# Kernel tuning notes

Hardware: AMD Instinct MI355X
Metric: run time of the kernel (lower is better)

The kernel has to match this reference:

```python
import jax, jax.numpy as jnp
import numpy as np

B, H, S_MAX, D = 2, 32, 8192, 128
S_NEW = 512

def setup_inputs() -> dict:
    key = jax.random.key(0)
    k1, k2 = jax.random.split(key)
    return {
        "input_pos": jnp.arange(S_NEW, dtype=jnp.int64 if jax.config.jax_enable_x64 else jnp.int32),
        "k_val": jax.random.normal(k1, (B, H, S_NEW, D), dtype=jnp.float32),
        "v_val": jax.random.normal(k2, (B, H, S_NEW, D), dtype=jnp.float32),
        "k_cache": jnp.zeros((B, H, S_MAX, D), dtype=jnp.float32),
        "kt_cache": jnp.zeros((B, H, D, S_MAX), dtype=jnp.float32),
        "v_cache": jnp.zeros((B, H, S_MAX, D), dtype=jnp.float32),
    }

def reference(input_pos, k_val, v_val, k_cache, kt_cache, v_cache):
    # Scatter-write new K/V (and K^T) into the caches at input_pos.
    k_out = k_cache.at[:, :, input_pos].set(k_val)                      # [B,H,S_max,D]
    kt_out = kt_cache.at[:, :, :, input_pos].set(
        jnp.swapaxes(k_val, -1, -2))                                    # [B,H,D,S_max]
    v_out = v_cache.at[:, :, input_pos].set(v_val)                      # [B,H,S_max,D]
    # Module returns (kt.transpose(-1,-2), k, v)
    return (jnp.swapaxes(kt_out, -1, -2), k_out, v_out)
```

## Files before the change

kernel.cpp:

```cpp
#include <hip/hip_runtime.h>


#define S_MAXC 8192
#define DC     128
#define BHC    64

__global__ void init_inv(int* __restrict__ inv) {
    int i = blockIdx.x * blockDim.x + threadIdx.x;
    if (i < S_MAXC) inv[i] = -1;
}

__global__ void scatter_inv(const int* __restrict__ pos, int* __restrict__ inv, int n) {
    int j = blockIdx.x * blockDim.x + threadIdx.x;
    if (j < n) inv[pos[j]] = j;
}

__global__ void __launch_bounds__(256) copy_scatter(
        const float4* __restrict__ k_val,
        const float4* __restrict__ v_val,
        const float4* __restrict__ k_cache,
        const float4* __restrict__ v_cache,
        const int*    __restrict__ inv,
        float4* __restrict__ out_k,
        float4* __restrict__ out_v,
        int s_new) {
    long i = (long)blockIdx.x * blockDim.x + threadIdx.x;
    int d4 = (int)(i & 31);
    int s  = (int)((i >> 5) & (S_MAXC - 1));
    int bh = (int)(i >> 18);
    int j = inv[s];
    if (j >= 0) {
        long src = ((long)bh * s_new + j) * 32 + d4;
        out_k[i] = k_val[src];
        out_v[i] = v_val[src];
    } else {
        out_k[i] = k_cache[i];
        out_v[i] = v_cache[i];
    }
}

__global__ void __launch_bounds__(256) transpose_kt(
        const float*  __restrict__ kt_cache,
        const float4* __restrict__ k_val,
        const int*    __restrict__ inv,
        float4* __restrict__ out0,
        int s_new) {
    __shared__ __align__(16) float tile[32][132];
    const int bh = blockIdx.y;
    const int s0 = blockIdx.x * 32;
    const int t  = threadIdx.x;
    const int q  = t & 7;
    const int r  = t >> 3;

    const float* ktb = kt_cache + (long)bh * DC * S_MAXC;
    #pragma unroll
    for (int p = 0; p < 4; ++p) {
        int d = p * 32 + r;
        float4 vld = *(const float4*)(ktb + (long)d * S_MAXC + s0 + 4 * q);
        tile[4 * q + 0][d] = vld.x;
        tile[4 * q + 1][d] = vld.y;
        tile[4 * q + 2][d] = vld.z;
        tile[4 * q + 3][d] = vld.w;
    }
    __syncthreads();

    const int sl = r;
    const int s  = s0 + sl;
    const int j  = inv[s];
    float4* outrow = out0 + ((long)bh * S_MAXC + s) * 32;
    if (j >= 0) {
        const float4* src = k_val + ((long)bh * s_new + j) * 32;
        #pragma unroll
        for (int m = 0; m < 4; ++m)
            outrow[q + 8 * m] = src[q + 8 * m];
    } else {
        #pragma unroll
        for (int m = 0; m < 4; ++m) {
            int dd = 4 * (q + 8 * m);
            outrow[q + 8 * m] = *(const float4*)&tile[sl][dd];
        }
    }
}

extern "C" void kernel_launch(void* const* d_in, const int* in_sizes, int n_in,
                              void* d_out, int out_size, void* d_ws, size_t ws_size,
                              hipStream_t stream) {
    const int*   input_pos = (const int*)  d_in[0];
    const float* k_val     = (const float*)d_in[1];
    const float* v_val     = (const float*)d_in[2];
    const float* k_cache   = (const float*)d_in[3];
    const float* kt_cache  = (const float*)d_in[4];
    const float* v_cache   = (const float*)d_in[5];
    const int s_new = in_sizes[0];

    const long per_out = (long)BHC * S_MAXC * DC;
    float* out0 = (float*)d_out;
    float* out1 = out0 + per_out;
    float* out2 = out1 + per_out;

    int* inv = (int*)d_ws;

    init_inv<<<S_MAXC / 256, 256, 0, stream>>>(inv);
    scatter_inv<<<(s_new + 255) / 256, 256, 0, stream>>>(input_pos, inv, s_new);

    const long total4 = per_out / 4;
    copy_scatter<<<(int)(total4 / 256), 256, 0, stream>>>(
        (const float4*)k_val, (const float4*)v_val,
        (const float4*)k_cache, (const float4*)v_cache, inv,
        (float4*)out1, (float4*)out2, s_new);

    dim3 grid_t(S_MAXC / 32, BHC);
    transpose_kt<<<grid_t, 256, 0, stream>>>(
        kt_cache, (const float4*)k_val, inv, (float4*)out0, s_new);
}
```

Measured before the change: 1.262 ms.

## Fuse K/V copy-scatter and K^T transpose into one kernel with nontemporal accesses

Merges the copy_scatter and transpose_kt kernels into a single kernel. Each 32-row tile now produces all three outputs: the transposed K^T, K and V. For scattered rows, k_val and v_val are read once and written to both K outputs. Cache loads and all output stores use nontemporal builtins to avoid polluting the cache on this purely streaming workload. The change saves a kernel launch and improves tail balance, but every block now needs more registers and does more work.

```diff
diff --git a/kernel.cpp b/kernel.cpp
--- a/kernel.cpp
+++ b/kernel.cpp
@@ -4,6 +4,8 @@
 #define S_MAXC 8192
 #define DC     128
 #define BHC    64
+
+typedef __attribute__((ext_vector_type(4))) float v4f;
 
 __global__ void init_inv(int* __restrict__ inv) {
     int i = blockIdx.x * blockDim.x + threadIdx.x;
@@ -15,48 +17,31 @@
     if (j < n) inv[pos[j]] = j;
 }
 
-__global__ void __launch_bounds__(256) copy_scatter(
-        const float4* __restrict__ k_val,
-        const float4* __restrict__ v_val,
-        const float4* __restrict__ k_cache,
-        const float4* __restrict__ v_cache,
-        const int*    __restrict__ inv,
-        float4* __restrict__ out_k,
-        float4* __restrict__ out_v,
-        int s_new) {
-    long i = (long)blockIdx.x * blockDim.x + threadIdx.x;
-    int d4 = (int)(i & 31);
-    int s  = (int)((i >> 5) & (S_MAXC - 1));
-    int bh = (int)(i >> 18);
-    int j = inv[s];
-    if (j >= 0) {
-        long src = ((long)bh * s_new + j) * 32 + d4;
-        out_k[i] = k_val[src];
-        out_v[i] = v_val[src];
-    } else {
-        out_k[i] = k_cache[i];
-        out_v[i] = v_cache[i];
-    }
-}
-
-__global__ void __launch_bounds__(256) transpose_kt(
-        const float*  __restrict__ kt_cache,
-        const float4* __restrict__ k_val,
-        const int*    __restrict__ inv,
-        float4* __restrict__ out0,
+__global__ void __launch_bounds__(256) fused_kv(
+        const v4f* __restrict__ k_val,
+        const v4f* __restrict__ v_val,
+        const v4f* __restrict__ k_cache,
+        const v4f* __restrict__ v_cache,
+        const float* __restrict__ kt_cache,
+        const int*  __restrict__ inv,
+        v4f* __restrict__ out0,
+        v4f* __restrict__ out1,
+        v4f* __restrict__ out2,
         int s_new) {
     __shared__ __align__(16) float tile[32][132];
-    const int bh = blockIdx.y;
-    const int s0 = blockIdx.x * 32;
-    const int t  = threadIdx.x;
-    const int q  = t & 7;
-    const int r  = t >> 3;
+    const int tid = blockIdx.x;
+    const int bh  = tid >> 8;
+    const int s0  = (tid & 255) << 5;
+    const int t   = threadIdx.x;
+    const int q   = t & 7;
+    const int r   = t >> 3;
 
     const float* ktb = kt_cache + (long)bh * DC * S_MAXC;
     #pragma unroll
     for (int p = 0; p < 4; ++p) {
         int d = p * 32 + r;
-        float4 vld = *(const float4*)(ktb + (long)d * S_MAXC + s0 + 4 * q);
+        v4f vld = __builtin_nontemporal_load(
+            (const v4f*)(ktb + (long)d * S_MAXC + s0 + 4 * q));
         tile[4 * q + 0][d] = vld.x;
         tile[4 * q + 1][d] = vld.y;
         tile[4 * q + 2][d] = vld.z;
@@ -64,20 +49,36 @@
     }
     __syncthreads();
 
-    const int sl = r;
-    const int s  = s0 + sl;
-    const int j  = inv[s];
-    float4* outrow = out0 + ((long)bh * S_MAXC + s) * 32;
+    const int s = s0 + r;
+    const int j = inv[s];
+    const long row = (long)bh * S_MAXC + s;
+    v4f* o0 = out0 + row * 32;
+    v4f* o1 = out1 + row * 32;
+    v4f* o2 = out2 + row * 32;
     if (j >= 0) {
-        const float4* src = k_val + ((long)bh * s_new + j) * 32;
-        #pragma unroll
-        for (int m = 0; m < 4; ++m)
-            outrow[q + 8 * m] = src[q + 8 * m];
-    } else {
+        const v4f* kv = k_val + ((long)bh * s_new + j) * 32;
+        const v4f* vv = v_val + ((long)bh * s_new + j) * 32;
         #pragma unroll
         for (int m = 0; m < 4; ++m) {
-            int dd = 4 * (q + 8 * m);
-            outrow[q + 8 * m] = *(const float4*)&tile[sl][dd];
+            int c = q + 8 * m;
+            v4f kx = kv[c];
+            v4f vx = vv[c];
+            __builtin_nontemporal_store(kx, o0 + c);
+            __builtin_nontemporal_store(kx, o1 + c);
+            __builtin_nontemporal_store(vx, o2 + c);
+        }
+    } else {
+        const v4f* kc = k_cache + row * 32;
+        const v4f* vc = v_cache + row * 32;
+        #pragma unroll
+        for (int m = 0; m < 4; ++m) {
+            int c = q + 8 * m;
+            v4f kx = __builtin_nontemporal_load(kc + c);
+            v4f vx = __builtin_nontemporal_load(vc + c);
+            v4f tx = *(const v4f*)&tile[r][4 * c];
+            __builtin_nontemporal_store(tx, o0 + c);
+            __builtin_nontemporal_store(kx, o1 + c);
+            __builtin_nontemporal_store(vx, o2 + c);
         }
     }
 }
@@ -103,13 +104,10 @@
     init_inv<<<S_MAXC / 256, 256, 0, stream>>>(inv);
     scatter_inv<<<(s_new + 255) / 256, 256, 0, stream>>>(input_pos, inv, s_new);
 
-    const long total4 = per_out / 4;
-    copy_scatter<<<(int)(total4 / 256), 256, 0, stream>>>(
-        (const float4*)k_val, (const float4*)v_val,
-        (const float4*)k_cache, (const float4*)v_cache, inv,
-        (float4*)out1, (float4*)out2, s_new);
-
-    dim3 grid_t(S_MAXC / 32, BHC);
-    transpose_kt<<<grid_t, 256, 0, stream>>>(
-        kt_cache, (const float4*)k_val, inv, (float4*)out0, s_new);
+    const int n_tiles = BHC * (S_MAXC / 32);
+    fused_kv<<<n_tiles, 256, 0, stream>>>(
+        (const v4f*)k_val, (const v4f*)v_val,
+        (const v4f*)k_cache, (const v4f*)v_cache,
+        kt_cache, inv,
+        (v4f*)out0, (v4f*)out1, (v4f*)out2, s_new);
 }
```

After: 1.255 ms. No clear change (-0.5%).
